# Kernel optimization log

Hardware: AMD Instinct MI355X
Metric: run time of the kernel (lower is better)

The kernel has to match this reference:

```python
import jax, jax.numpy as jnp
import numpy as np

INF = 100000.0


def setup_inputs() -> dict:
    key = jax.random.key(0)
    k1, k2, k3 = jax.random.split(key, 3)
    B, W, T, S, D = 64, 32, 256, 128, 64
    query = jax.random.normal(k1, (S, D), dtype=jnp.float32)
    keys = jax.random.normal(k2, (B, W, T, D), dtype=jnp.float32)
    values = jax.random.normal(k3, (B, W, T, D), dtype=jnp.float32)
    return {"query": query, "keys": keys, "values": values}


def reference(query, keys, values):
    # p: [B, W, S, T] = broadcasted query @ keys^T
    p = jnp.einsum("sd,bwtd->bwst", query, keys)
    # zero scores are masked out with -INF before softmax
    mask = jnp.where(p == 0, -INF, 0.0).astype(p.dtype)
    attn = jax.nn.softmax(p + mask, axis=-1)
    # outputs: [B, W, S, Dv]
    return jnp.einsum("bwst,bwtv->bwsv", attn, values)
```

## Files before the change

kernel.cpp:

```cpp
#include <hip/hip_runtime.h>

typedef _Float16 h16;
typedef __attribute__((ext_vector_type(4))) _Float16 half4v;
typedef __attribute__((ext_vector_type(8))) _Float16 half8v;
typedef __attribute__((ext_vector_type(4))) float f32x4;

static constexpr int Tn = 256;
static constexpr int Dn = 64;
static constexpr int Sn = 128;
static constexpr int KSTR = 72;
static constexpr int VSTR = 264;
static constexpr int PSTR = 40;

#define MFMA_F16 __builtin_amdgcn_mfma_f32_16x16x32_f16

__global__ __launch_bounds__(256, 2)
void attn_kernel(const float* __restrict__ Q, const float* __restrict__ K,
                 const float* __restrict__ V, float* __restrict__ O)
{
    __shared__ __align__(16) h16 KV[Tn * KSTR];
    __shared__ __align__(16) h16 Pb[4 * 2 * 32 * PSTR];

    const int head = blockIdx.x;
    const int tid  = threadIdx.x;
    const int wave = tid >> 6;
    const int lane = tid & 63;
    const int quad = lane >> 4;
    const int l16  = lane & 15;

    const float* __restrict__ Kh = K + (size_t)head * (Tn * Dn);
    const float* __restrict__ Vh = V + (size_t)head * (Tn * Dn);
    float* __restrict__ Oh       = O + (size_t)head * (Sn * Dn);

    half8v qf[2][2];
#pragma unroll
    for (int m = 0; m < 2; ++m) {
        const float* qrow = Q + (wave * 32 + m * 16 + l16) * Dn;
#pragma unroll
        for (int kt = 0; kt < 2; ++kt) {
            float4 a = *reinterpret_cast<const float4*>(qrow + kt * 32 + quad * 8);
            float4 b = *reinterpret_cast<const float4*>(qrow + kt * 32 + quad * 8 + 4);
            half8v f;
            f[0] = (h16)a.x; f[1] = (h16)a.y; f[2] = (h16)a.z; f[3] = (h16)a.w;
            f[4] = (h16)b.x; f[5] = (h16)b.y; f[6] = (h16)b.z; f[7] = (h16)b.w;
            qf[m][kt] = f;
        }
    }

#pragma unroll
    for (int it = 0; it < 16; ++it) {
        int f   = it * 256 + tid;
        int row = f >> 4;
        int c4  = (f & 15) << 2;
        float4 kv = *reinterpret_cast<const float4*>(Kh + row * Dn + c4);
        half4v hv;
        hv[0] = (h16)kv.x; hv[1] = (h16)kv.y; hv[2] = (h16)kv.z; hv[3] = (h16)kv.w;
        *reinterpret_cast<half4v*>(&KV[row * KSTR + c4]) = hv;
    }
    __syncthreads();

    f32x4 acc[2][16] = {};
#pragma unroll
    for (int n = 0; n < 16; ++n) {
#pragma unroll
        for (int kt = 0; kt < 2; ++kt) {
            half8v bf = *reinterpret_cast<const half8v*>(
                &KV[(n * 16 + l16) * KSTR + kt * 32 + quad * 8]);
            acc[0][n] = MFMA_F16(qf[0][kt], bf, acc[0][n], 0, 0, 0);
            acc[1][n] = MFMA_F16(qf[1][kt], bf, acc[1][n], 0, 0, 0);
        }
    }

    float rinv[2][4];
#pragma unroll
    for (int m = 0; m < 2; ++m) {
#pragma unroll
        for (int r = 0; r < 4; ++r) {
            float mx = -3.0e38f;
#pragma unroll
            for (int n = 0; n < 16; ++n) {
                float p = acc[m][n][r];
                p = (p == 0.0f) ? -100000.0f : p;
                acc[m][n][r] = p;
                mx = fmaxf(mx, p);
            }
            mx = fmaxf(mx, __shfl_xor(mx, 1));
            mx = fmaxf(mx, __shfl_xor(mx, 2));
            mx = fmaxf(mx, __shfl_xor(mx, 4));
            mx = fmaxf(mx, __shfl_xor(mx, 8));
            float sm = 0.0f;
#pragma unroll
            for (int n = 0; n < 16; ++n) {
                float e = __expf(acc[m][n][r] - mx);
                acc[m][n][r] = e;
                sm += e;
            }
            sm += __shfl_xor(sm, 1);
            sm += __shfl_xor(sm, 2);
            sm += __shfl_xor(sm, 4);
            sm += __shfl_xor(sm, 8);
            rinv[m][r] = 1.0f / sm;
        }
    }

    __syncthreads();
#pragma unroll
    for (int i = 0; i < 16; ++i) {
        int dbase = (i >> 2) * 16 + quad * 4;
        int t     = ((i & 3) * 4 + wave) * 16 + l16;
        float4 vv = *reinterpret_cast<const float4*>(Vh + t * Dn + dbase);
        int ts = t ^ (quad << 3);
        KV[(dbase + 0) * VSTR + ts] = (h16)vv.x;
        KV[(dbase + 1) * VSTR + ts] = (h16)vv.y;
        KV[(dbase + 2) * VSTR + ts] = (h16)vv.z;
        KV[(dbase + 3) * VSTR + ts] = (h16)vv.w;
    }
    __syncthreads();

    f32x4 oacc[2][4] = {};
    h16* Pw = &Pb[wave * 2 * 32 * PSTR];
#pragma unroll
    for (int c = 0; c < 8; ++c) {
        h16* buf = Pw + (c & 1) * 32 * PSTR;
#pragma unroll
        for (int m = 0; m < 2; ++m)
#pragma unroll
            for (int nn = 0; nn < 2; ++nn) {
                int n = 2 * c + nn;
#pragma unroll
                for (int r = 0; r < 4; ++r) {
                    int row = m * 16 + quad * 4 + r;
                    int col = (nn * 16 + l16) ^ (quad << 3);
                    buf[row * PSTR + col] = (h16)acc[m][n][r];
                }
            }
        asm volatile("s_waitcnt lgkmcnt(0)" ::: "memory");
        half8v pa[2];
#pragma unroll
        for (int m = 0; m < 2; ++m)
            pa[m] = *reinterpret_cast<const half8v*>(
                &buf[(m * 16 + l16) * PSTR + ((quad ^ (l16 >> 2)) << 3)]);
#pragma unroll
        for (int dt = 0; dt < 4; ++dt) {
            half8v vb = *reinterpret_cast<const half8v*>(
                &KV[(dt * 16 + l16) * VSTR + c * 32 + ((quad ^ (l16 >> 2)) << 3)]);
            oacc[0][dt] = MFMA_F16(pa[0], vb, oacc[0][dt], 0, 0, 0);
            oacc[1][dt] = MFMA_F16(pa[1], vb, oacc[1][dt], 0, 0, 0);
        }
    }

#pragma unroll
    for (int m = 0; m < 2; ++m)
#pragma unroll
        for (int dt = 0; dt < 4; ++dt)
#pragma unroll
            for (int r = 0; r < 4; ++r) {
                int s = wave * 32 + m * 16 + quad * 4 + r;
                Oh[s * Dn + dt * 16 + l16] = oacc[m][dt][r] * rinv[m][r];
            }
}

extern "C" void kernel_launch(void* const* d_in, const int* in_sizes, int n_in,
                              void* d_out, int out_size, void* d_ws, size_t ws_size,
                              hipStream_t stream) {
    (void)n_in; (void)out_size; (void)d_ws; (void)ws_size;
    const float* q = (const float*)d_in[0];
    const float* k = (const float*)d_in[1];
    const float* v = (const float*)d_in[2];
    float* o = (float*)d_out;
    const int heads = in_sizes[1] / (Tn * Dn);
    attn_kernel<<<dim3(heads), dim3(256), 0, stream>>>(q, k, v, o);
}
```

Measured before the change: 302.3 us.

## Stream V in chunks into LDS overlapped with QK^T MFMA

V is prefetched into registers 64 tokens at a time while the QK^T MFMAs for the matching K rows run. Each chunk is then written, transposed to fp16, into the LDS region those K rows just freed, using a chunked layout with the K stride. The aim is to hide global V load latency behind the score computation instead of loading V only after softmax. The cost is extra barriers per chunk and more live registers for the prefetch buffer.

Measured after the change: 299.6 us. Within noise of the previous version (-0.9%).

```diff
diff --git a/kernel.cpp b/kernel.cpp
--- a/kernel.cpp
+++ b/kernel.cpp
@@ -9,8 +9,8 @@
 static constexpr int Dn = 64;
 static constexpr int Sn = 128;
 static constexpr int KSTR = 72;
-static constexpr int VSTR = 264;
 static constexpr int PSTR = 40;
+static constexpr int VCH  = 64 * KSTR;
 
 #define MFMA_F16 __builtin_amdgcn_mfma_f32_16x16x32_f16
 
@@ -60,60 +60,85 @@
     __syncthreads();
 
     f32x4 acc[2][16] = {};
+    float rinv[2][4];
+    float4 vreg[4];
+
 #pragma unroll
-    for (int n = 0; n < 16; ++n) {
-#pragma unroll
-        for (int kt = 0; kt < 2; ++kt) {
-            half8v bf = *reinterpret_cast<const half8v*>(
-                &KV[(n * 16 + l16) * KSTR + kt * 32 + quad * 8]);
-            acc[0][n] = MFMA_F16(qf[0][kt], bf, acc[0][n], 0, 0, 0);
-            acc[1][n] = MFMA_F16(qf[1][kt], bf, acc[1][n], 0, 0, 0);
-        }
+    for (int j = 0; j < 4; ++j) {
+        int t     = 0 * 64 + wave * 16 + l16;
+        int dbase = j * 16 + quad * 4;
+        vreg[j] = *reinterpret_cast<const float4*>(Vh + t * Dn + dbase);
     }
 
-    float rinv[2][4];
 #pragma unroll
-    for (int m = 0; m < 2; ++m) {
+    for (int c = 0; c < 4; ++c) {
 #pragma unroll
-        for (int r = 0; r < 4; ++r) {
-            float mx = -3.0e38f;
+        for (int nn = 0; nn < 4; ++nn) {
+            int n = c * 4 + nn;
 #pragma unroll
-            for (int n = 0; n < 16; ++n) {
-                float p = acc[m][n][r];
-                p = (p == 0.0f) ? -100000.0f : p;
-                acc[m][n][r] = p;
-                mx = fmaxf(mx, p);
+            for (int kt = 0; kt < 2; ++kt) {
+                half8v bf = *reinterpret_cast<const half8v*>(
+                    &KV[(n * 16 + l16) * KSTR + kt * 32 + quad * 8]);
+                acc[0][n] = MFMA_F16(qf[0][kt], bf, acc[0][n], 0, 0, 0);
+                acc[1][n] = MFMA_F16(qf[1][kt], bf, acc[1][n], 0, 0, 0);
             }
-            mx = fmaxf(mx, __shfl_xor(mx, 1));
-            mx = fmaxf(mx, __shfl_xor(mx, 2));
-            mx = fmaxf(mx, __shfl_xor(mx, 4));
-            mx = fmaxf(mx, __shfl_xor(mx, 8));
-            float sm = 0.0f;
+        }
+
+        if (c == 3) {
 #pragma unroll
-            for (int n = 0; n < 16; ++n) {
-                float e = __expf(acc[m][n][r] - mx);
-                acc[m][n][r] = e;
-                sm += e;
+            for (int m = 0; m < 2; ++m) {
+#pragma unroll
+                for (int r = 0; r < 4; ++r) {
+                    float mx = -3.0e38f;
+#pragma unroll
+                    for (int n = 0; n < 16; ++n) {
+                        float p = acc[m][n][r];
+                        p = (p == 0.0f) ? -100000.0f : p;
+                        acc[m][n][r] = p;
+                        mx = fmaxf(mx, p);
+                    }
+                    mx = fmaxf(mx, __shfl_xor(mx, 1));
+                    mx = fmaxf(mx, __shfl_xor(mx, 2));
+                    mx = fmaxf(mx, __shfl_xor(mx, 4));
+                    mx = fmaxf(mx, __shfl_xor(mx, 8));
+                    float sm = 0.0f;
+#pragma unroll
+                    for (int n = 0; n < 16; ++n) {
+                        float e = __expf(acc[m][n][r] - mx);
+                        acc[m][n][r] = e;
+                        sm += e;
+                    }
+                    sm += __shfl_xor(sm, 1);
+                    sm += __shfl_xor(sm, 2);
+                    sm += __shfl_xor(sm, 4);
+                    sm += __shfl_xor(sm, 8);
+                    rinv[m][r] = 1.0f / sm;
+                }
             }
-            sm += __shfl_xor(sm, 1);
-            sm += __shfl_xor(sm, 2);
-            sm += __shfl_xor(sm, 4);
-            sm += __shfl_xor(sm, 8);
-            rinv[m][r] = 1.0f / sm;
         }
-    }
 
-    __syncthreads();
+        __syncthreads();
+
 #pragma unroll
-    for (int i = 0; i < 16; ++i) {
-        int dbase = (i >> 2) * 16 + quad * 4;
-        int t     = ((i & 3) * 4 + wave) * 16 + l16;
-        float4 vv = *reinterpret_cast<const float4*>(Vh + t * Dn + dbase);
-        int ts = t ^ (quad << 3);
-        KV[(dbase + 0) * VSTR + ts] = (h16)vv.x;
-        KV[(dbase + 1) * VSTR + ts] = (h16)vv.y;
-        KV[(dbase + 2) * VSTR + ts] = (h16)vv.z;
-        KV[(dbase + 3) * VSTR + ts] = (h16)vv.w;
+        for (int j = 0; j < 4; ++j) {
+            int dbase = j * 16 + quad * 4;
+            int trel  = wave * 16 + l16;
+            int tc    = trel ^ (quad << 3);
+            float4 vv = vreg[j];
+            KV[c * VCH + (dbase + 0) * KSTR + tc] = (h16)vv.x;
+            KV[c * VCH + (dbase + 1) * KSTR + tc] = (h16)vv.y;
+            KV[c * VCH + (dbase + 2) * KSTR + tc] = (h16)vv.z;
+            KV[c * VCH + (dbase + 3) * KSTR + tc] = (h16)vv.w;
+        }
+
+        if (c < 3) {
+#pragma unroll
+            for (int j = 0; j < 4; ++j) {
+                int t     = (c + 1) * 64 + wave * 16 + l16;
+                int dbase = j * 16 + quad * 4;
+                vreg[j] = *reinterpret_cast<const float4*>(Vh + t * Dn + dbase);
+            }
+        }
     }
     __syncthreads();
 
@@ -143,7 +168,8 @@
 #pragma unroll
         for (int dt = 0; dt < 4; ++dt) {
             half8v vb = *reinterpret_cast<const half8v*>(
-                &KV[(dt * 16 + l16) * VSTR + c * 32 + ((quad ^ (l16 >> 2)) << 3)]);
+                &KV[(c >> 1) * VCH + (dt * 16 + l16) * KSTR + (c & 1) * 32 +
+                    ((quad ^ (l16 >> 2)) << 3)]);
             oacc[0][dt] = MFMA_F16(pa[0], vb, oacc[0][dt], 0, 0, 0);
             oacc[1][dt] = MFMA_F16(pa[1], vb, oacc[1][dt], 0, 0, 0);
         }
```

## Split each head's query rows across two blocks and rechunk V layout

Applied to the files above, without the earlier changes.

Launches two blocks per head, each covering 64 of the 128 query rows, so each wave does one 16-row M tile instead of two. This cuts register pressure so occupancy can rise (launch bounds raised to 3), and doubles the grid for better CU fill. V is now stored transposed in 64-token chunks reusing the K stride, and the P staging buffer shrinks to a single buffer. The cost is that K and V are loaded and converted twice per head, doubling global reads, and the removed double-buffering of P may add LDS hazards between iterations.

After: 303.9 us. No clear change (+0.5%).

```diff
diff --git a/kernel.cpp b/kernel.cpp
--- a/kernel.cpp
+++ b/kernel.cpp
@@ -9,33 +9,33 @@
 static constexpr int Dn = 64;
 static constexpr int Sn = 128;
 static constexpr int KSTR = 72;
-static constexpr int VSTR = 264;
 static constexpr int PSTR = 40;
+static constexpr int VCH  = 64 * KSTR;
 
 #define MFMA_F16 __builtin_amdgcn_mfma_f32_16x16x32_f16
 
-__global__ __launch_bounds__(256, 2)
+__global__ __launch_bounds__(256, 3)
 void attn_kernel(const float* __restrict__ Q, const float* __restrict__ K,
                  const float* __restrict__ V, float* __restrict__ O)
 {
     __shared__ __align__(16) h16 KV[Tn * KSTR];
-    __shared__ __align__(16) h16 Pb[4 * 2 * 32 * PSTR];
+    __shared__ __align__(16) h16 Pb[4 * 16 * PSTR];
 
-    const int head = blockIdx.x;
-    const int tid  = threadIdx.x;
-    const int wave = tid >> 6;
-    const int lane = tid & 63;
-    const int quad = lane >> 4;
-    const int l16  = lane & 15;
+    const int head  = blockIdx.x >> 1;
+    const int shalf = blockIdx.x & 1;
+    const int tid   = threadIdx.x;
+    const int wave  = tid >> 6;
+    const int lane  = tid & 63;
+    const int quad  = lane >> 4;
+    const int l16   = lane & 15;
 
     const float* __restrict__ Kh = K + (size_t)head * (Tn * Dn);
     const float* __restrict__ Vh = V + (size_t)head * (Tn * Dn);
     float* __restrict__ Oh       = O + (size_t)head * (Sn * Dn);
 
-    half8v qf[2][2];
-#pragma unroll
-    for (int m = 0; m < 2; ++m) {
-        const float* qrow = Q + (wave * 32 + m * 16 + l16) * Dn;
+    half8v qf[2];
+    {
+        const float* qrow = Q + (shalf * 64 + wave * 16 + l16) * Dn;
 #pragma unroll
         for (int kt = 0; kt < 2; ++kt) {
             float4 a = *reinterpret_cast<const float4*>(qrow + kt * 32 + quad * 8);
@@ -43,7 +43,7 @@
             half8v f;
             f[0] = (h16)a.x; f[1] = (h16)a.y; f[2] = (h16)a.z; f[3] = (h16)a.w;
             f[4] = (h16)b.x; f[5] = (h16)b.y; f[6] = (h16)b.z; f[7] = (h16)b.w;
-            qf[m][kt] = f;
+            qf[kt] = f;
         }
     }
 
@@ -59,48 +59,44 @@
     }
     __syncthreads();
 
-    f32x4 acc[2][16] = {};
+    f32x4 acc[16] = {};
 #pragma unroll
     for (int n = 0; n < 16; ++n) {
 #pragma unroll
         for (int kt = 0; kt < 2; ++kt) {
             half8v bf = *reinterpret_cast<const half8v*>(
                 &KV[(n * 16 + l16) * KSTR + kt * 32 + quad * 8]);
-            acc[0][n] = MFMA_F16(qf[0][kt], bf, acc[0][n], 0, 0, 0);
-            acc[1][n] = MFMA_F16(qf[1][kt], bf, acc[1][n], 0, 0, 0);
+            acc[n] = MFMA_F16(qf[kt], bf, acc[n], 0, 0, 0);
         }
     }
 
-    float rinv[2][4];
+    float rinv[4];
 #pragma unroll
-    for (int m = 0; m < 2; ++m) {
+    for (int r = 0; r < 4; ++r) {
+        float mx = -3.0e38f;
 #pragma unroll
-        for (int r = 0; r < 4; ++r) {
-            float mx = -3.0e38f;
+        for (int n = 0; n < 16; ++n) {
+            float p = acc[n][r];
+            p = (p == 0.0f) ? -100000.0f : p;
+            acc[n][r] = p;
+            mx = fmaxf(mx, p);
+        }
+        mx = fmaxf(mx, __shfl_xor(mx, 1));
+        mx = fmaxf(mx, __shfl_xor(mx, 2));
+        mx = fmaxf(mx, __shfl_xor(mx, 4));
+        mx = fmaxf(mx, __shfl_xor(mx, 8));
+        float sm = 0.0f;
 #pragma unroll
-            for (int n = 0; n < 16; ++n) {
-                float p = acc[m][n][r];
-                p = (p == 0.0f) ? -100000.0f : p;
-                acc[m][n][r] = p;
-                mx = fmaxf(mx, p);
-            }
-            mx = fmaxf(mx, __shfl_xor(mx, 1));
-            mx = fmaxf(mx, __shfl_xor(mx, 2));
-            mx = fmaxf(mx, __shfl_xor(mx, 4));
-            mx = fmaxf(mx, __shfl_xor(mx, 8));
-            float sm = 0.0f;
-#pragma unroll
-            for (int n = 0; n < 16; ++n) {
-                float e = __expf(acc[m][n][r] - mx);
-                acc[m][n][r] = e;
-                sm += e;
-            }
-            sm += __shfl_xor(sm, 1);
-            sm += __shfl_xor(sm, 2);
-            sm += __shfl_xor(sm, 4);
-            sm += __shfl_xor(sm, 8);
-            rinv[m][r] = 1.0f / sm;
+        for (int n = 0; n < 16; ++n) {
+            float e = __expf(acc[n][r] - mx);
+            acc[n][r] = e;
+            sm += e;
         }
+        sm += __shfl_xor(sm, 1);
+        sm += __shfl_xor(sm, 2);
+        sm += __shfl_xor(sm, 4);
+        sm += __shfl_xor(sm, 8);
+        rinv[r] = 1.0f / sm;
     }
 
     __syncthreads();
@@ -109,55 +105,48 @@
         int dbase = (i >> 2) * 16 + quad * 4;
         int t     = ((i & 3) * 4 + wave) * 16 + l16;
         float4 vv = *reinterpret_cast<const float4*>(Vh + t * Dn + dbase);
-        int ts = t ^ (quad << 3);
-        KV[(dbase + 0) * VSTR + ts] = (h16)vv.x;
-        KV[(dbase + 1) * VSTR + ts] = (h16)vv.y;
-        KV[(dbase + 2) * VSTR + ts] = (h16)vv.z;
-        KV[(dbase + 3) * VSTR + ts] = (h16)vv.w;
+        int c  = t >> 6;
+        int tc = (t & 63) ^ (quad << 3);
+        KV[c * VCH + (dbase + 0) * KSTR + tc] = (h16)vv.x;
+        KV[c * VCH + (dbase + 1) * KSTR + tc] = (h16)vv.y;
+        KV[c * VCH + (dbase + 2) * KSTR + tc] = (h16)vv.z;
+        KV[c * VCH + (dbase + 3) * KSTR + tc] = (h16)vv.w;
     }
     __syncthreads();
 
-    f32x4 oacc[2][4] = {};
-    h16* Pw = &Pb[wave * 2 * 32 * PSTR];
+    f32x4 oacc[4] = {};
+    h16* buf = &Pb[wave * 16 * PSTR];
 #pragma unroll
     for (int c = 0; c < 8; ++c) {
-        h16* buf = Pw + (c & 1) * 32 * PSTR;
 #pragma unroll
-        for (int m = 0; m < 2; ++m)
+        for (int nn = 0; nn < 2; ++nn) {
+            int n = 2 * c + nn;
 #pragma unroll
-            for (int nn = 0; nn < 2; ++nn) {
-                int n = 2 * c + nn;
-#pragma unroll
-                for (int r = 0; r < 4; ++r) {
-                    int row = m * 16 + quad * 4 + r;
-                    int col = (nn * 16 + l16) ^ (quad << 3);
-                    buf[row * PSTR + col] = (h16)acc[m][n][r];
-                }
+            for (int r = 0; r < 4; ++r) {
+                int row = quad * 4 + r;
+                int col = (nn * 16 + l16) ^ (quad << 3);
+                buf[row * PSTR + col] = (h16)acc[n][r];
             }
+        }
         asm volatile("s_waitcnt lgkmcnt(0)" ::: "memory");
-        half8v pa[2];
-#pragma unroll
-        for (int m = 0; m < 2; ++m)
-            pa[m] = *reinterpret_cast<const half8v*>(
-                &buf[(m * 16 + l16) * PSTR + ((quad ^ (l16 >> 2)) << 3)]);
+        half8v pa = *reinterpret_cast<const half8v*>(
+            &buf[l16 * PSTR + ((quad ^ (l16 >> 2)) << 3)]);
 #pragma unroll
         for (int dt = 0; dt < 4; ++dt) {
             half8v vb = *reinterpret_cast<const half8v*>(
-                &KV[(dt * 16 + l16) * VSTR + c * 32 + ((quad ^ (l16 >> 2)) << 3)]);
-            oacc[0][dt] = MFMA_F16(pa[0], vb, oacc[0][dt], 0, 0, 0);
-            oacc[1][dt] = MFMA_F16(pa[1], vb, oacc[1][dt], 0, 0, 0);
+                &KV[(c >> 1) * VCH + (dt * 16 + l16) * KSTR + (c & 1) * 32 +
+                    ((quad ^ (l16 >> 2)) << 3)]);
+            oacc[dt] = MFMA_F16(pa, vb, oacc[dt], 0, 0, 0);
         }
     }
 
 #pragma unroll
-    for (int m = 0; m < 2; ++m)
+    for (int dt = 0; dt < 4; ++dt)
 #pragma unroll
-        for (int dt = 0; dt < 4; ++dt)
-#pragma unroll
-            for (int r = 0; r < 4; ++r) {
-                int s = wave * 32 + m * 16 + quad * 4 + r;
-                Oh[s * Dn + dt * 16 + l16] = oacc[m][dt][r] * rinv[m][r];
-            }
+        for (int r = 0; r < 4; ++r) {
+            int s = shalf * 64 + wave * 16 + quad * 4 + r;
+            Oh[s * Dn + dt * 16 + l16] = oacc[dt][r] * rinv[r];
+        }
 }
 
 extern "C" void kernel_launch(void* const* d_in, const int* in_sizes, int n_in,
@@ -169,5 +158,5 @@
     const float* v = (const float*)d_in[2];
     float* o = (float*)d_out;
     const int heads = in_sizes[1] / (Tn * Dn);
-    attn_kernel<<<dim3(heads), dim3(256), 0, stream>>>(q, k, v, o);
+    attn_kernel<<<dim3(heads * 2), dim3(256), 0, stream>>>(q, k, v, o);
 }
```
